# Kernel tuning notes

Hardware: AMD Instinct MI355X
Metric: run time of the kernel (lower is better)

## Reference

```python
import jax, jax.numpy as jnp
import numpy as np

H = 8  # heads hardcoded in LightGFormer


def layernorm(x, g, b, eps=1e-5):
    m = x.mean(-1, keepdims=True)
    v = ((x - m) ** 2).mean(-1, keepdims=True)
    return (x - m) / jnp.sqrt(v + eps) * g + b


def setup_inputs() -> dict:
    key = jax.random.key(0)
    B, N, D, L = 16, 512, 256, 4
    Dff = 4 * D
    ks = jax.random.split(key, 12)

    def w(k, shape, scale=0.02):
        return jax.random.normal(k, shape, jnp.float32) * scale

    return {
        "input": w(ks[0], (B, N, D), 1.0),
        "input_v": w(ks[1], (B, N, D), 1.0),
        "pos_emb": w(ks[2], (N, D)),
        "Wq": w(ks[3], (L, D, D)), "bq": jnp.zeros((L, D), jnp.float32),
        "Wk": w(ks[4], (L, D, D)), "bk": jnp.zeros((L, D), jnp.float32),
        "Wv": w(ks[5], (L, D, D)), "bv": jnp.zeros((L, D), jnp.float32),
        "Wo": w(ks[6], (L, D, D)), "bo": jnp.zeros((L, D), jnp.float32),
        "W1": w(ks[7], (L, D, Dff)), "b1": jnp.zeros((L, Dff), jnp.float32),
        "W2": w(ks[8], (L, Dff // 2, D // 2)), "b2": jnp.zeros((L, D // 2), jnp.float32),
        "g1": jnp.ones((L, D), jnp.float32), "be1": jnp.zeros((L, D), jnp.float32),
        "g2": jnp.ones((L, D), jnp.float32), "be2": jnp.zeros((L, D), jnp.float32),
        "gf": jnp.ones((D,), jnp.float32), "bf": jnp.zeros((D,), jnp.float32),
        "mask": jax.random.randint(ks[9], (N, N), 0, 2) > 0,
    }


def reference(input, input_v, pos_emb, Wq, bq, Wk, bk, Wv, bv, Wo, bo,
              W1, b1, W2, b2, g1, be1, g2, be2, gf, bf, mask):
    B, N, D = input.shape
    L = Wq.shape[0]
    dk = D // H
    scale = 1.0 / float(np.sqrt(dk))

    x = input + pos_emb[None]       # learned positional encoding
    xv = input_v + pos_emb[None]    # values stream (never updated across layers)

    for i in range(L):
        # --- self-attention: queries/keys from x, values from xv ---
        q = (x @ Wq[i] + bq[i]).reshape(B, N, H, dk)
        k = (x @ Wk[i] + bk[i]).reshape(B, N, H, dk)
        v = (xv @ Wv[i] + bv[i]).reshape(B, N, H, dk)
        att = jnp.einsum('bqhd,bkhd->bhqk', q, k) * scale
        if i % 2 == 1:  # odd layers use the mask (Lightformer alternation)
            att = jnp.where(mask[None, None], -jnp.inf, att)
        att = jax.nn.softmax(att, axis=-1)
        o = jnp.einsum('bhqk,bkhd->bqhd', att, v).reshape(B, N, D)
        o = o @ Wo[i] + bo[i]
        x = layernorm(x + o, g1[i], be1[i])
        # --- FFN with grouped second linear: [.., 2, 2D] @ [2D, D/2] ---
        h = jax.nn.gelu(x @ W1[i] + b1[i], approximate=False)
        h = (h.reshape(B, N, 2, 2 * D) @ W2[i] + b2[i]).reshape(B, N, D)
        x = layernorm(x + h, g2[i], be2[i])

    x = layernorm(x, gf, bf)  # final attention_norm
    return x
```

## Files before the change

kernel.cpp:

```cpp
#include <hip/hip_runtime.h>
#include <hip/hip_bf16.h>
#include <math.h>

#define BDIM 16
#define NSEQ 512
#define DMODEL 256
#define NLAYER 4
#define NHEAD 8
#define DK 32
#define DFF 1024
#define BN (BDIM * NSEQ)
#define ND (NSEQ * DMODEL)

typedef __bf16 bf16x8 __attribute__((ext_vector_type(8)));
typedef float floatx4 __attribute__((ext_vector_type(4)));
typedef unsigned uint32x2 __attribute__((ext_vector_type(2)));

static __device__ __forceinline__ unsigned short f2bf(float f) {
    unsigned u = __float_as_uint(f);
    unsigned r = (u + 0x7FFFu + ((u >> 16) & 1u)) >> 16;
    return (unsigned short)r;
}
static __device__ __forceinline__ float bf2f(unsigned short u) {
    return __uint_as_float(((unsigned)u) << 16);
}

static __device__ __forceinline__ void async_ld16(const unsigned short* g,
                                                  unsigned short* l) {
    __builtin_amdgcn_global_load_lds(
        (const __attribute__((address_space(1))) unsigned int*)g,
        (__attribute__((address_space(3))) unsigned int*)l, 16, 0, 0);
}

static __device__ __forceinline__ float gelu_f(float c) {
    float u = 0.7978845608028654f * (c + 0.044715f * c * c * c);
    return c * (1.f / (1.f + __expf(-2.f * u)));
}

static __device__ __forceinline__ unsigned cvtpk(float lo, float hi) {
    unsigned r;
    asm("v_cvt_pk_bf16_f32 %0, %1, %2" : "=v"(r) : "v"(lo), "v"(hi));
    return r;
}

__global__ void conv_all_kernel(const float* __restrict__ Wq, const float* __restrict__ Wk,
                                const float* __restrict__ Wv, const float* __restrict__ Wo,
                                const float* __restrict__ W1, const float* __restrict__ W2,
                                const int* __restrict__ mask,
                                unsigned short* __restrict__ wqT, unsigned short* __restrict__ wkT,
                                unsigned short* __restrict__ wvT,
                                unsigned short* __restrict__ wo_s,
                                unsigned short* __restrict__ w1_s, unsigned short* __restrict__ w2_s,
                                unsigned* __restrict__ bits) {
    int blk = blockIdx.x, tid = threadIdx.x;
    if (blk < 3072) {
        int i = blk * 256 + tid;
        int sel = i >> 18;
        int j = i & 262143;
        int l = j >> 16, rem = j & 65535, kk = rem >> 8, n = rem & 255;
        const float* src = sel == 0 ? Wq : sel == 1 ? Wk : Wv;
        unsigned short* dst = sel == 0 ? wqT : sel == 1 ? wkT : wvT;
        dst[(size_t)l * 65536 + n * 256 + kk] = f2bf(src[j]);
    } else if (blk < 4096) {
        int i = (blk - 3072) * 256 + tid;
        int l = i >> 16, o = i & 65535;
        int j = o & 7, quad = (o >> 3) & 3, l16 = (o >> 5) & 15;
        int kt = (o >> 9) & 7, cg = (o >> 12) & 15;
        int k = kt * 32 + (j >> 2) * 16 + quad * 4 + (j & 3);
        int dout = cg * 16 + l16;
        wo_s[(size_t)l * 65536 + o] = f2bf(Wo[(size_t)l * 65536 + k * 256 + dout]);
    } else if (blk < 8192) {
        int i = (blk - 4096) * 256 + tid;
        int l = i >> 18, o = i & 262143;
        int j = o & 7, quad = (o >> 3) & 3, l16 = (o >> 5) & 15;
        int kt = (o >> 9) & 7, cg = (o >> 12) & 63;
        int k = kt * 32 + (j >> 2) * 16 + quad * 4 + (j & 3);
        int dout = cg * 16 + l16;
        w1_s[(size_t)l * 262144 + o] = f2bf(W1[(size_t)l * 262144 + k * 1024 + dout]);
    } else if (blk < 9216) {
        int i = (blk - 8192) * 256 + tid;
        int l = i >> 16, o = i & 65535;
        int j = o & 7, quad = (o >> 3) & 3, l16 = (o >> 5) & 15;
        int kt = (o >> 9) & 15, cg = (o >> 13) & 7;
        int k = kt * 32 + (j >> 2) * 16 + quad * 4 + (j & 3);
        int dout = cg * 16 + l16;
        w2_s[(size_t)l * 65536 + o] = f2bf(W2[(size_t)l * 65536 + k * 128 + dout]);
    } else {
        int w = (blk - 9216) * 256 + tid;
        int r = w >> 4, wi = w & 15;
        const int* src = mask + r * NSEQ + wi * 32;
        unsigned acc = 0;
#pragma unroll
        for (int j = 0; j < 32; j++) acc |= (src[j] != 0 ? 1u : 0u) << j;
        bits[w] = acc;
    }
}

__global__ void add_pos_kernel(const float* __restrict__ in,
                               const float* __restrict__ inv,
                               const float* __restrict__ pos,
                               float* __restrict__ x,
                               unsigned short* __restrict__ xb,
                               unsigned short* __restrict__ xvb,
                               int total) {
    int i = blockIdx.x * blockDim.x + threadIdx.x;
    if (i < total) {
        float pe = pos[i % ND];
        float a = in[i] + pe;
        float b = inv[i] + pe;
        x[i] = a;
        xb[i] = f2bf(a);
        xvb[i] = f2bf(b);
    }
}

__global__ __launch_bounds__(256) void qkv_mfma_kernel(
        const unsigned short* __restrict__ xb,
        const unsigned short* __restrict__ xvb,
        const unsigned short* __restrict__ WqT, const unsigned short* __restrict__ WkT,
        const unsigned short* __restrict__ WvT,
        const float* __restrict__ bq, const float* __restrict__ bk,
        const float* __restrict__ bv,
        unsigned short* __restrict__ qo, unsigned short* __restrict__ ko,
        unsigned short* __restrict__ vo) {
    int proj = blockIdx.x >> 1;
    const unsigned short* A  = (proj == 2) ? xvb : xb;
    const unsigned short* Bt = (proj == 0) ? WqT : (proj == 1) ? WkT : WvT;
    const float* bias        = (proj == 0) ? bq  : (proj == 1) ? bk  : bv;
    unsigned short* Cb       = (proj == 0) ? qo  : (proj == 1) ? ko  : vo;
    float qscale = (proj == 0) ? 0.17677669529663687f : 1.f;

    __shared__ unsigned short As[128 * 32];
    __shared__ unsigned short Bs[128 * 32];
    int tid = threadIdx.x;
    int wave = tid >> 6, lane = tid & 63;
    int rowBase = blockIdx.y * 128, colBase = (blockIdx.x & 1) * 128;
    int m0w = (wave & 1) * 64, n0w = (wave >> 1) * 64;
    int lr = lane & 15, quad = lane >> 4;
    int qx = quad ^ (lr & 3);

    floatx4 acc[4][4];
#pragma unroll
    for (int mi = 0; mi < 4; mi++)
#pragma unroll
        for (int nj = 0; nj < 4; nj++) acc[mi][nj] = (floatx4)0.0f;

    for (int kt = 0; kt < DMODEL; kt += 32) {
#pragma unroll
        for (int t = 0; t < 2; t++) {
            int idx = t * 256 + tid;
            int row = idx >> 2, kv8 = ((idx ^ row) & 3) * 8;
            async_ld16(A + (size_t)(rowBase + row) * DMODEL + kt + kv8, &As[idx * 8]);
            async_ld16(Bt + (size_t)(colBase + row) * DMODEL + kt + kv8, &Bs[idx * 8]);
        }
        __syncthreads();
        bf16x8 af[4], bfr[4];
#pragma unroll
        for (int mi = 0; mi < 4; mi++)
            af[mi] = *(const bf16x8*)&As[(m0w + mi * 16 + lr) * 32 + qx * 8];
#pragma unroll
        for (int nj = 0; nj < 4; nj++)
            bfr[nj] = *(const bf16x8*)&Bs[(n0w + nj * 16 + lr) * 32 + qx * 8];
#pragma unroll
        for (int mi = 0; mi < 4; mi++)
#pragma unroll
            for (int nj = 0; nj < 4; nj++)
                acc[mi][nj] = __builtin_amdgcn_mfma_f32_16x16x32_bf16(
                    af[mi], bfr[nj], acc[mi][nj], 0, 0, 0);
        __syncthreads();
    }

#pragma unroll
    for (int mi = 0; mi < 4; mi++) {
#pragma unroll
        for (int r = 0; r < 4; r++) {
            int grow = rowBase + m0w + mi * 16 + quad * 4 + r;
#pragma unroll
            for (int nj = 0; nj < 4; nj++) {
                int gcol = colBase + n0w + nj * 16 + lr;
                float c = (acc[mi][nj][r] + bias[gcol]) * qscale;
                size_t off = ((size_t)((grow >> 9) * 8 + (gcol >> 5)) << 14)
                           + (size_t)(grow & 511) * 32 + (gcol & 31);
                Cb[off] = f2bf(c);
            }
        }
    }
}

__global__ __launch_bounds__(512, 4) void ffn_fused_kernel(
        const unsigned short* __restrict__ ab_f,
        const unsigned short* __restrict__ wo_s,
        const unsigned short* __restrict__ w1_s,
        const unsigned short* __restrict__ w2_s,
        const float* __restrict__ bo,
        const float* __restrict__ g1, const float* __restrict__ be1,
        const float* __restrict__ b1,
        const float* __restrict__ b2,
        const float* __restrict__ g2, const float* __restrict__ be2,
        const float* __restrict__ gf, const float* __restrict__ bf_,
        float* __restrict__ xf, unsigned short* __restrict__ xb,
        float* __restrict__ outF, int finalize) {
    __shared__ unsigned short X1s[8 * 512];
    __shared__ unsigned short Hs[16 * 512];
    __shared__ float redA[16][8], redB[16][8];
    __shared__ float redC[16][8], redD[16][8];
    __shared__ float redE[16][8], redF[16][8];

    int tid = threadIdx.x;
    int w = tid >> 6, lane = tid & 63, l16 = lane & 15, quad = lane >> 4;
    int bid = blockIdx.x;
    int rowBase = bid * 16;
    int fo = (l16 * 4 + quad) * 8;

#define TR2(d0, d1, addr)                                                  \
    asm volatile("ds_read_b64_tr_b16 %0, %2\n\t"                           \
                 "ds_read_b64_tr_b16 %1, %2 offset:512"                    \
                 : "=&v"(d0), "=&v"(d1) : "v"(addr))

    float bo_r[2], g1_r[2], be1_r[2], g2_r[2], be2_r[2], gf_r[2], bfr_[2];
#pragma unroll
    for (int cg = 0; cg < 2; cg++) {
        int colA = w * 32 + cg * 16 + l16;
        bo_r[cg] = bo[colA]; g1_r[cg] = g1[colA]; be1_r[cg] = be1[colA];
        int colC = cg * 128 + w * 16 + l16;
        g2_r[cg] = g2[colC]; be2_r[cg] = be2[colC];
        gf_r[cg] = gf[colC]; bfr_[cg] = bf_[colC];
    }
    float b1_r[2][4];
#pragma unroll
    for (int g = 0; g < 2; g++)
#pragma unroll
        for (int c = 0; c < 4; c++)
            b1_r[g][c] = b1[g * 512 + w * 64 + c * 16 + l16];
    float b2_r = b2[w * 16 + l16];
    float x0r[4][2];
#pragma unroll
    for (int r = 0; r < 4; r++)
#pragma unroll
        for (int cg = 0; cg < 2; cg++)
            x0r[r][cg] = xf[(size_t)(rowBase + quad * 4 + r) * 256 + w * 32 + cg * 16 + l16];

    floatx4 accA[2];
    accA[0] = (floatx4)0.0f; accA[1] = (floatx4)0.0f;

    bf16x8 afQ[4], bwQ[4][2];
#pragma unroll
    for (int p = 0; p < 4; p++) {
        afQ[p] = *(const bf16x8*)(ab_f + ((size_t)bid * 8 + p) * 512 + fo);
#pragma unroll
        for (int cg = 0; cg < 2; cg++)
            bwQ[p][cg] = *(const bf16x8*)(wo_s + ((size_t)((w * 2 + cg) * 8 + p)) * 512 + fo);
    }

#pragma unroll
    for (int kt = 0; kt < 8; kt++) {
        int sl = kt & 3;
#pragma unroll
        for (int cg = 0; cg < 2; cg++)
            accA[cg] = __builtin_amdgcn_mfma_f32_16x16x32_bf16(afQ[sl], bwQ[sl][cg], accA[cg], 0, 0, 0);
        if (kt < 4) {
            afQ[sl] = *(const bf16x8*)(ab_f + ((size_t)bid * 8 + kt + 4) * 512 + fo);
#pragma unroll
            for (int cg = 0; cg < 2; cg++)
                bwQ[sl][cg] = *(const bf16x8*)(wo_s + ((size_t)((w * 2 + cg) * 8 + kt + 4)) * 512 + fo);
        }
    }

#pragma unroll
    for (int r = 0; r < 4; r++) {
        int tok = quad * 4 + r;
        float s = 0.f, s2 = 0.f;
#pragma unroll
        for (int cg = 0; cg < 2; cg++) {
            float v = accA[cg][r] + bo_r[cg] + x0r[r][cg];
            accA[cg][r] = v; s += v; s2 += v * v;
        }
#pragma unroll
        for (int off = 1; off <= 8; off <<= 1) {
            s += __shfl_xor(s, off);
            s2 += __shfl_xor(s2, off);
        }
        if (l16 == 0) { redA[tok][w] = s; redB[tok][w] = s2; }
    }
    __syncthreads();
#pragma unroll
    for (int r = 0; r < 4; r++) {
        int tok = quad * 4 + r;
        float ts = 0.f, tq = 0.f;
#pragma unroll
        for (int ww = 0; ww < 8; ww++) { ts += redA[tok][ww]; tq += redB[tok][ww]; }
        float mean = ts * (1.f / 256.f);
        float var = tq * (1.f / 256.f) - mean * mean;
        float rstd = rsqrtf(var + 1e-5f);
#pragma unroll
        for (int cg = 0; cg < 2; cg++)
            accA[cg][r] = (accA[cg][r] - mean) * rstd * g1_r[cg] + be1_r[cg];
    }
#pragma unroll
    for (int cg = 0; cg < 2; cg++) {
        uint32x2 pk;
        pk[0] = cvtpk(accA[cg][0], accA[cg][1]);
        pk[1] = cvtpk(accA[cg][2], accA[cg][3]);
        *(uint32x2*)&X1s[w * 512 + (cg * 16 + l16) * 16 + quad * 4] = pk;
    }
    __syncthreads();

    unsigned x1addr = (unsigned)(size_t)&X1s[0] + (unsigned)(lane * 8);
    unsigned haddr  = (unsigned)(size_t)&Hs[0]  + (unsigned)(lane * 8);

    floatx4 y[2];
    y[0] = (floatx4)0.0f; y[1] = (floatx4)0.0f;

#pragma unroll
    for (int g = 0; g < 2; g++) {
        floatx4 accB[4];
#pragma unroll
        for (int c = 0; c < 4; c++) accB[c] = (floatx4)0.0f;

        uint32x2 tA0, tA1, tB0, tB1;
        TR2(tA0, tA1, x1addr);
        TR2(tB0, tB1, x1addr + 1024u);
        bf16x8 bwB[2][4];
#pragma unroll
        for (int p = 0; p < 2; p++)
#pragma unroll
            for (int c = 0; c < 4; c++)
                bwB[p][c] = *(const bf16x8*)(w1_s +
                    ((size_t)((g * 32 + w * 4 + c) * 8 + p)) * 512 + fo);

#pragma unroll
        for (int kt = 0; kt < 8; kt++) {
            if (kt < 7) asm volatile("s_waitcnt lgkmcnt(2)");
            else        asm volatile("s_waitcnt lgkmcnt(0)");
            __builtin_amdgcn_sched_barrier(0);
            union { bf16x8 v8; uint32x2 u[2]; } afu;
            if ((kt & 1) == 0) { afu.u[0] = tA0; afu.u[1] = tA1; }
            else               { afu.u[0] = tB0; afu.u[1] = tB1; }
            if (kt < 6) {
                if ((kt & 1) == 0) TR2(tA0, tA1, x1addr + (unsigned)((kt + 2) * 1024));
                else               TR2(tB0, tB1, x1addr + (unsigned)((kt + 2) * 1024));
            }
            int sl = kt & 1;
#pragma unroll
            for (int c = 0; c < 4; c++)
                accB[c] = __builtin_amdgcn_mfma_f32_16x16x32_bf16(afu.v8, bwB[sl][c], accB[c], 0, 0, 0);
            if (kt < 6) {
#pragma unroll
                for (int c = 0; c < 4; c++)
                    bwB[sl][c] = *(const bf16x8*)(w1_s +
                        ((size_t)((g * 32 + w * 4 + c) * 8 + kt + 2)) * 512 + fo);
            }
        }
#pragma unroll
        for (int c = 0; c < 4; c++) {
            float bb = b1_r[g][c];
            float o0 = gelu_f(accB[c][0] + bb);
            float o1 = gelu_f(accB[c][1] + bb);
            float o2 = gelu_f(accB[c][2] + bb);
            float o3 = gelu_f(accB[c][3] + bb);
            int ct = w * 2 + (c >> 1), colL = (c & 1) * 16 + l16;
            uint32x2 pk;
            pk[0] = cvtpk(o0, o1);
            pk[1] = cvtpk(o2, o3);
            *(uint32x2*)&Hs[ct * 512 + colL * 16 + quad * 4] = pk;
        }
        __syncthreads();

        TR2(tA0, tA1, haddr);
        TR2(tB0, tB1, haddr + 1024u);
        bf16x8 bwC[4];
#pragma unroll
        for (int p = 0; p < 4; p++)
            bwC[p] = *(const bf16x8*)(w2_s + ((size_t)(w * 16 + p)) * 512 + fo);

#pragma unroll
        for (int kt = 0; kt < 16; kt++) {
            if (kt < 15) asm volatile("s_waitcnt lgkmcnt(2)");
            else         asm volatile("s_waitcnt lgkmcnt(0)");
            __builtin_amdgcn_sched_barrier(0);
            union { bf16x8 v8; uint32x2 u[2]; } afu;
            if ((kt & 1) == 0) { afu.u[0] = tA0; afu.u[1] = tA1; }
            else               { afu.u[0] = tB0; afu.u[1] = tB1; }
            if (kt < 14) {
                if ((kt & 1) == 0) TR2(tA0, tA1, haddr + (unsigned)((kt + 2) * 1024));
                else               TR2(tB0, tB1, haddr + (unsigned)((kt + 2) * 1024));
            }
            y[g] = __builtin_amdgcn_mfma_f32_16x16x32_bf16(afu.v8, bwC[kt & 3], y[g], 0, 0, 0);
            if (kt < 12)
                bwC[kt & 3] = *(const bf16x8*)(w2_s + ((size_t)(w * 16 + kt + 4)) * 512 + fo);
        }
        if (g == 0) __syncthreads();
    }
#undef TR2

#pragma unroll
    for (int r = 0; r < 4; r++) {
        int tok = quad * 4 + r;
        float s = 0.f, s2 = 0.f;
#pragma unroll
        for (int g = 0; g < 2; g++) {
            int col = g * 128 + w * 16 + l16;
            float x1v = bf2f(X1s[(col >> 5) * 512 + (col & 31) * 16 + tok]);
            float v = y[g][r] + b2_r + x1v;
            y[g][r] = v; s += v; s2 += v * v;
        }
#pragma unroll
        for (int off = 1; off <= 8; off <<= 1) {
            s += __shfl_xor(s, off);
            s2 += __shfl_xor(s2, off);
        }
        if (l16 == 0) { redC[tok][w] = s; redD[tok][w] = s2; }
    }
    __syncthreads();

    if (!finalize) {
#pragma unroll
        for (int r = 0; r < 4; r++) {
            int tok = quad * 4 + r;
            float ts = 0.f, tq = 0.f;
#pragma unroll
            for (int ww = 0; ww < 8; ww++) { ts += redC[tok][ww]; tq += redD[tok][ww]; }
            float mean = ts * (1.f / 256.f);
            float var = tq * (1.f / 256.f) - mean * mean;
            float rstd = rsqrtf(var + 1e-5f);
#pragma unroll
            for (int g = 0; g < 2; g++) {
                int col = g * 128 + w * 16 + l16;
                float o = (y[g][r] - mean) * rstd * g2_r[g] + be2_r[g];
                xf[(size_t)(rowBase + tok) * 256 + col] = o;
                xb[(size_t)(rowBase + tok) * 256 + col] = f2bf(o);
            }
        }
    } else {
#pragma unroll
        for (int r = 0; r < 4; r++) {
            int tok = quad * 4 + r;
            float ts = 0.f, tq = 0.f;
#pragma unroll
            for (int ww = 0; ww < 8; ww++) { ts += redC[tok][ww]; tq += redD[tok][ww]; }
            float mean = ts * (1.f / 256.f);
            float var = tq * (1.f / 256.f) - mean * mean;
            float rstd = rsqrtf(var + 1e-5f);
            float s3 = 0.f, q3 = 0.f;
#pragma unroll
            for (int g = 0; g < 2; g++) {
                float o = (y[g][r] - mean) * rstd * g2_r[g] + be2_r[g];
                y[g][r] = o; s3 += o; q3 += o * o;
            }
#pragma unroll
            for (int off = 1; off <= 8; off <<= 1) {
                s3 += __shfl_xor(s3, off);
                q3 += __shfl_xor(q3, off);
            }
            if (l16 == 0) { redE[tok][w] = s3; redF[tok][w] = q3; }
        }
        __syncthreads();
#pragma unroll
        for (int r = 0; r < 4; r++) {
            int tok = quad * 4 + r;
            float ts = 0.f, tq = 0.f;
#pragma unroll
            for (int ww = 0; ww < 8; ww++) { ts += redE[tok][ww]; tq += redF[tok][ww]; }
            float mean = ts * (1.f / 256.f);
            float var = tq * (1.f / 256.f) - mean * mean;
            float rstd = rsqrtf(var + 1e-5f);
#pragma unroll
            for (int g = 0; g < 2; g++) {
                int col = g * 128 + w * 16 + l16;
                outF[(size_t)(rowBase + tok) * 256 + col]
                    = (y[g][r] - mean) * rstd * gf_r[g] + bfr_[g];
            }
        }
    }
}

__global__ __launch_bounds__(256, 4) void attn_mfma_kernel(
        const unsigned short* __restrict__ q, const unsigned short* __restrict__ k,
        const unsigned short* __restrict__ v, unsigned short* __restrict__ ab_f,
        const unsigned* __restrict__ mbits_g, int use_mask) {
    int bid = blockIdx.x;
    int qg = bid >> 7;
    int bh = bid & 127;
    int h = bh & 7, b = bh >> 3;
    int tid = threadIdx.x;

    __shared__ unsigned short Vs[2][NSEQ * 16];

    const unsigned short* kbase = k + (size_t)(b * 8 + h) * (NSEQ * DK);
    const unsigned short* vbase = v + (size_t)(b * 8 + h) * (NSEQ * DK);

#pragma unroll
    for (int db = 0; db < 2; db++) {
#pragma unroll
        for (int t = 0; t < 4; t++) {
            int c = t * 256 + tid;
            int kk = c >> 1, half = c & 1;
            async_ld16(vbase + (size_t)kk * 32 + db * 16 + half * 8,
                       &Vs[db][c * 8]);
        }
    }

    int wave = tid >> 6, lane = tid & 63, l16 = lane & 15, quad = lane >> 4;
    int qbase = qg * 64 + wave * 16;

    bf16x8 qf = *(const bf16x8*)(q + ((size_t)(b * 8 + h) * NSEQ + qbase + l16) * 32 + quad * 8);

    unsigned mw[16];
    if (use_mask) {
        const uint4* mr = (const uint4*)(mbits_g + (size_t)(qbase + l16) * 16);
#pragma unroll
        for (int w = 0; w < 4; w++) *(uint4*)&mw[w * 4] = mr[w];
    } else {
#pragma unroll
        for (int w = 0; w < 16; w++) mw[w] = 0;
    }
    __syncthreads();

    unsigned va0 = (unsigned)(size_t)&Vs[0][0] + (unsigned)(lane * 8);
    unsigned va1 = (unsigned)(size_t)&Vs[1][0] + (unsigned)(lane * 8);

    const unsigned short* kfrag = kbase + (size_t)l16 * DK + quad * 8;

    floatx4 oT0 = (floatx4)0.f, oT1 = (floatx4)0.f;
    float m_run = -INFINITY, l_part = 0.f;

    uint32x2 t00, t01, t02, t03, t10, t11, t12, t13;
#define TR_ISSUE8(cp)                                                      \
    asm volatile("ds_read_b64_tr_b16 %0, %8\n\t"                           \
                 "ds_read_b64_tr_b16 %1, %8 offset:512\n\t"                \
                 "ds_read_b64_tr_b16 %2, %8 offset:1024\n\t"               \
                 "ds_read_b64_tr_b16 %3, %8 offset:1536\n\t"               \
                 "ds_read_b64_tr_b16 %4, %9\n\t"                           \
                 "ds_read_b64_tr_b16 %5, %9 offset:512\n\t"                \
                 "ds_read_b64_tr_b16 %6, %9 offset:1024\n\t"               \
                 "ds_read_b64_tr_b16 %7, %9 offset:1536"                   \
                 : "=&v"(t00), "=&v"(t01), "=&v"(t02), "=&v"(t03),         \
                   "=&v"(t10), "=&v"(t11), "=&v"(t12), "=&v"(t13)          \
                 : "v"(va0 + (unsigned)((cp) * 2048)),                     \
                   "v"(va1 + (unsigned)((cp) * 2048)))
    TR_ISSUE8(0);

    bf16x8 k0 = *(const bf16x8*)(kfrag);
    bf16x8 k1 = *(const bf16x8*)(kfrag + 16 * DK);
    bf16x8 k2 = *(const bf16x8*)(kfrag + 32 * DK);
    bf16x8 k3 = *(const bf16x8*)(kfrag + 48 * DK);

#pragma unroll
    for (int cp = 0; cp < 8; cp++) {
        floatx4 s0 = __builtin_amdgcn_mfma_f32_16x16x32_bf16(k0, qf, (floatx4)0.f, 0, 0, 0);
        floatx4 s1 = __builtin_amdgcn_mfma_f32_16x16x32_bf16(k1, qf, (floatx4)0.f, 0, 0, 0);
        floatx4 s2 = __builtin_amdgcn_mfma_f32_16x16x32_bf16(k2, qf, (floatx4)0.f, 0, 0, 0);
        floatx4 s3 = __builtin_amdgcn_mfma_f32_16x16x32_bf16(k3, qf, (floatx4)0.f, 0, 0, 0);

        bf16x8 k0n, k1n, k2n, k3n;
        if (cp < 7) {
            const unsigned short* kn = kfrag + (size_t)((cp + 1) * 64) * DK;
            k0n = *(const bf16x8*)(kn);
            k1n = *(const bf16x8*)(kn + 16 * DK);
            k2n = *(const bf16x8*)(kn + 32 * DK);
            k3n = *(const bf16x8*)(kn + 48 * DK);
        }

        float sv[16];
#pragma unroll
        for (int r = 0; r < 4; r++) {
            sv[r] = s0[r]; sv[4 + r] = s1[r];
            sv[8 + r] = s2[r]; sv[12 + r] = s3[r];
        }
        if (use_mask) {
            unsigned wb0 = mw[2 * cp], wb1 = mw[2 * cp + 1];
#pragma unroll
            for (int r = 0; r < 4; r++) {
                if ((wb0 >> (quad * 4 + r)) & 1)        sv[r]      = -INFINITY;
                if ((wb0 >> (16 + quad * 4 + r)) & 1)   sv[4 + r]  = -INFINITY;
                if ((wb1 >> (quad * 4 + r)) & 1)        sv[8 + r]  = -INFINITY;
                if ((wb1 >> (16 + quad * 4 + r)) & 1)   sv[12 + r] = -INFINITY;
            }
        }
        float mx = sv[0];
#pragma unroll
        for (int j = 1; j < 16; j++) mx = fmaxf(mx, sv[j]);
        mx = fmaxf(mx, __shfl_xor(mx, 16));
        mx = fmaxf(mx, __shfl_xor(mx, 32));
        if (!__all(mx <= m_run)) {
            float mnew = fmaxf(m_run, mx);
            float corr = (m_run == mnew) ? 1.f : __expf(m_run - mnew);
            l_part *= corr;
            oT0 *= corr; oT1 *= corr;
            m_run = mnew;
        }
        float p[16];
#pragma unroll
        for (int j = 0; j < 16; j++) {
            float e = __expf(sv[j] - m_run);
            p[j] = (sv[j] > -INFINITY) ? e : 0.f;
            l_part += p[j];
        }
        union { bf16x8 v8; unsigned u[4]; } pf0, pf1;
#pragma unroll
        for (int j = 0; j < 4; j++) {
            pf0.u[j] = cvtpk(p[2 * j], p[2 * j + 1]);
            pf1.u[j] = cvtpk(p[8 + 2 * j], p[8 + 2 * j + 1]);
        }

        asm volatile("s_waitcnt lgkmcnt(0)");
        __builtin_amdgcn_sched_barrier(0);
        union { bf16x8 v8; uint32x2 u[2]; } av0, av1, av2, av3;
        av0.u[0] = t00; av0.u[1] = t01;
        av2.u[0] = t02; av2.u[1] = t03;
        av1.u[0] = t10; av1.u[1] = t11;
        av3.u[0] = t12; av3.u[1] = t13;

        oT0 = __builtin_amdgcn_mfma_f32_16x16x32_bf16(av0.v8, pf0.v8, oT0, 0, 0, 0);
        oT1 = __builtin_amdgcn_mfma_f32_16x16x32_bf16(av1.v8, pf0.v8, oT1, 0, 0, 0);
        oT0 = __builtin_amdgcn_mfma_f32_16x16x32_bf16(av2.v8, pf1.v8, oT0, 0, 0, 0);
        oT1 = __builtin_amdgcn_mfma_f32_16x16x32_bf16(av3.v8, pf1.v8, oT1, 0, 0, 0);
        if (cp < 7) TR_ISSUE8(cp + 1);
        k0 = k0n; k1 = k1n; k2 = k2n; k3 = k3n;
    }
#undef TR_ISSUE8

    float l = l_part;
    l += __shfl_xor(l, 16);
    l += __shfl_xor(l, 32);
    float invl = (l > 0.f) ? 1.f / l : 0.f;

    uint4 val;
    val.x = cvtpk(oT0[0] * invl, oT0[1] * invl);
    val.y = cvtpk(oT0[2] * invl, oT0[3] * invl);
    val.z = cvtpk(oT1[0] * invl, oT1[1] * invl);
    val.w = cvtpk(oT1[2] * invl, oT1[3] * invl);
    size_t panel = (size_t)b * 32 + qg * 4 + wave;
    *(uint4*)(ab_f + (panel * 8 + h) * 512 + (l16 * 4 + quad) * 8) = val;
}

extern "C" void kernel_launch(void* const* d_in, const int* in_sizes, int n_in,
                              void* d_out, int out_size, void* d_ws, size_t ws_size,
                              hipStream_t stream) {
    const float* input  = (const float*)d_in[0];
    const float* inputv = (const float*)d_in[1];
    const float* pos    = (const float*)d_in[2];
    const float* Wq = (const float*)d_in[3];
    const float* bq = (const float*)d_in[4];
    const float* Wk = (const float*)d_in[5];
    const float* bk = (const float*)d_in[6];
    const float* Wv = (const float*)d_in[7];
    const float* bv = (const float*)d_in[8];
    const float* Wo = (const float*)d_in[9];
    const float* bo = (const float*)d_in[10];
    const float* W1 = (const float*)d_in[11];
    const float* b1 = (const float*)d_in[12];
    const float* W2 = (const float*)d_in[13];
    const float* b2 = (const float*)d_in[14];
    const float* g1 = (const float*)d_in[15];
    const float* be1 = (const float*)d_in[16];
    const float* g2 = (const float*)d_in[17];
    const float* be2 = (const float*)d_in[18];
    const float* gf = (const float*)d_in[19];
    const float* bff = (const float*)d_in[20];
    const int* mask = (const int*)d_in[21];

    float* out = (float*)d_out;

    char* wsb = (char*)d_ws;
    float* x_f  = (float*)(wsb + ((size_t)0 << 20));
    unsigned short* x_b  = (unsigned short*)(wsb + ((size_t)8 << 20));
    unsigned short* xv_b = (unsigned short*)(wsb + ((size_t)12 << 20));
    unsigned short* qb_b = (unsigned short*)(wsb + ((size_t)16 << 20));
    unsigned short* kb_b = (unsigned short*)(wsb + ((size_t)20 << 20));
    unsigned short* vb_b = (unsigned short*)(wsb + ((size_t)24 << 20));
    unsigned short* ab_f = (unsigned short*)(wsb + ((size_t)28 << 20));
    unsigned short* wqT = (unsigned short*)(wsb + ((size_t)32 << 20));
    unsigned short* wkT = wqT + (size_t)4 * 65536;
    unsigned short* wvT = wkT + (size_t)4 * 65536;
    unsigned short* wo_s = wvT + (size_t)4 * 65536;
    unsigned short* w1_s = wo_s + (size_t)4 * 65536;
    unsigned short* w2_s = w1_s + (size_t)4 * 262144;
    unsigned* mbits = (unsigned*)(wsb + ((size_t)37 << 20));

    const size_t TOK = (size_t)BN * DMODEL;

    conv_all_kernel<<<9248, 256, 0, stream>>>(Wq, Wk, Wv, Wo, W1, W2, mask,
                                              wqT, wkT, wvT, wo_s, w1_s, w2_s, mbits);
    add_pos_kernel<<<(int)((TOK + 255) / 256), 256, 0, stream>>>(
        input, inputv, pos, x_f, x_b, xv_b, (int)TOK);

    for (int i = 0; i < NLAYER; i++) {
        const unsigned short* WqT_i = wqT + (size_t)i * 65536;
        const unsigned short* WkT_i = wkT + (size_t)i * 65536;
        const unsigned short* WvT_i = wvT + (size_t)i * 65536;
        const unsigned short* Wo_i  = wo_s + (size_t)i * 65536;
        const unsigned short* W1_i  = w1_s + (size_t)i * 262144;
        const unsigned short* W2_i  = w2_s + (size_t)i * 65536;

        qkv_mfma_kernel<<<dim3(6, 64), 256, 0, stream>>>(
            x_b, xv_b, WqT_i, WkT_i, WvT_i,
            bq + i * DMODEL, bk + i * DMODEL, bv + i * DMODEL,
            qb_b, kb_b, vb_b);

        attn_mfma_kernel<<<BDIM * NHEAD * 8, 256, 0, stream>>>(
            qb_b, kb_b, vb_b, ab_f, mbits, (i & 1));

        ffn_fused_kernel<<<BN / 16, 512, 0, stream>>>(
            ab_f, Wo_i, W1_i, W2_i,
            bo + i * DMODEL, g1 + i * DMODEL, be1 + i * DMODEL,
            b1 + i * DFF, b2 + i * (DMODEL / 2),
            g2 + i * DMODEL, be2 + i * DMODEL,
            gf, bff, x_f, x_b, out, (i == NLAYER - 1) ? 1 : 0);
    }
}
```

Before: 376.2 us.

## Store activations and QKV weights in MFMA fragment layout and drop LDS staging

Activations (x_b, xv_b) and the Q/K/V weights are now written in a pre-swizzled MFMA fragment order. This lets the QKV projection load operands straight from global memory into registers, with no LDS staging and no barriers. The QKV kernel moves from 128x128 tiles to one 16-token panel per block, giving 1536 blocks with a register double-buffered K loop. The cost is that every block re-reads its weight columns from L2, and the FFN epilogue now does an extra pass, including a redundant zero write, to scatter x_b in the new layout.

```diff
diff --git a/kernel.cpp b/kernel.cpp
--- a/kernel.cpp
+++ b/kernel.cpp
@@ -43,12 +43,20 @@
     return r;
 }
 
+static __device__ __forceinline__ size_t fd_addr(int tok, int col) {
+    int panel = tok >> 4, l16 = tok & 15;
+    int kt = col >> 5, kp = col & 31;
+    int quad = (kp >> 2) & 3;
+    int j = (kp & 3) + 4 * ((kp >> 4) & 1);
+    return ((size_t)(panel * 8 + kt) << 9) + (l16 * 4 + quad) * 8 + j;
+}
+
 __global__ void conv_all_kernel(const float* __restrict__ Wq, const float* __restrict__ Wk,
                                 const float* __restrict__ Wv, const float* __restrict__ Wo,
                                 const float* __restrict__ W1, const float* __restrict__ W2,
                                 const int* __restrict__ mask,
-                                unsigned short* __restrict__ wqT, unsigned short* __restrict__ wkT,
-                                unsigned short* __restrict__ wvT,
+                                unsigned short* __restrict__ wq_s, unsigned short* __restrict__ wk_s,
+                                unsigned short* __restrict__ wv_s,
                                 unsigned short* __restrict__ wo_s,
                                 unsigned short* __restrict__ w1_s, unsigned short* __restrict__ w2_s,
                                 unsigned* __restrict__ bits) {
@@ -56,11 +64,15 @@
     if (blk < 3072) {
         int i = blk * 256 + tid;
         int sel = i >> 18;
-        int j = i & 262143;
-        int l = j >> 16, rem = j & 65535, kk = rem >> 8, n = rem & 255;
+        int jj = i & 262143;
+        int l = jj >> 16, o = jj & 65535;
+        int j = o & 7, quad = (o >> 3) & 3, l16 = (o >> 5) & 15;
+        int kt = (o >> 9) & 7, cg = (o >> 12) & 15;
+        int k = kt * 32 + (j >> 2) * 16 + quad * 4 + (j & 3);
+        int dout = cg * 16 + l16;
         const float* src = sel == 0 ? Wq : sel == 1 ? Wk : Wv;
-        unsigned short* dst = sel == 0 ? wqT : sel == 1 ? wkT : wvT;
-        dst[(size_t)l * 65536 + n * 256 + kk] = f2bf(src[j]);
+        unsigned short* dst = sel == 0 ? wq_s : sel == 1 ? wk_s : wv_s;
+        dst[(size_t)l * 65536 + o] = f2bf(src[(size_t)l * 65536 + k * 256 + dout]);
     } else if (blk < 4096) {
         int i = (blk - 3072) * 256 + tid;
         int l = i >> 16, o = i & 65535;
@@ -109,80 +121,71 @@
         float a = in[i] + pe;
         float b = inv[i] + pe;
         x[i] = a;
-        xb[i] = f2bf(a);
-        xvb[i] = f2bf(b);
+        size_t fa = fd_addr(i >> 8, i & 255);
+        xb[fa] = f2bf(a);
+        xvb[fa] = f2bf(b);
     }
 }
 
 __global__ __launch_bounds__(256) void qkv_mfma_kernel(
-        const unsigned short* __restrict__ xb,
-        const unsigned short* __restrict__ xvb,
-        const unsigned short* __restrict__ WqT, const unsigned short* __restrict__ WkT,
-        const unsigned short* __restrict__ WvT,
+        const unsigned short* __restrict__ xb_f,
+        const unsigned short* __restrict__ xvb_f,
+        const unsigned short* __restrict__ wq_s, const unsigned short* __restrict__ wk_s,
+        const unsigned short* __restrict__ wv_s,
         const float* __restrict__ bq, const float* __restrict__ bk,
         const float* __restrict__ bv,
         unsigned short* __restrict__ qo, unsigned short* __restrict__ ko,
         unsigned short* __restrict__ vo) {
-    int proj = blockIdx.x >> 1;
-    const unsigned short* A  = (proj == 2) ? xvb : xb;
-    const unsigned short* Bt = (proj == 0) ? WqT : (proj == 1) ? WkT : WvT;
+    int bx = blockIdx.x;
+    int proj = bx >> 9, panel = bx & 511;
+    const unsigned short* A  = (proj == 2) ? xvb_f : xb_f;
+    const unsigned short* W  = (proj == 0) ? wq_s : (proj == 1) ? wk_s : wv_s;
     const float* bias        = (proj == 0) ? bq  : (proj == 1) ? bk  : bv;
     unsigned short* Cb       = (proj == 0) ? qo  : (proj == 1) ? ko  : vo;
     float qscale = (proj == 0) ? 0.17677669529663687f : 1.f;
 
-    __shared__ unsigned short As[128 * 32];
-    __shared__ unsigned short Bs[128 * 32];
     int tid = threadIdx.x;
-    int wave = tid >> 6, lane = tid & 63;
-    int rowBase = blockIdx.y * 128, colBase = (blockIdx.x & 1) * 128;
-    int m0w = (wave & 1) * 64, n0w = (wave >> 1) * 64;
-    int lr = lane & 15, quad = lane >> 4;
-    int qx = quad ^ (lr & 3);
-
-    floatx4 acc[4][4];
-#pragma unroll
-    for (int mi = 0; mi < 4; mi++)
-#pragma unroll
-        for (int nj = 0; nj < 4; nj++) acc[mi][nj] = (floatx4)0.0f;
-
-    for (int kt = 0; kt < DMODEL; kt += 32) {
-#pragma unroll
-        for (int t = 0; t < 2; t++) {
-            int idx = t * 256 + tid;
-            int row = idx >> 2, kv8 = ((idx ^ row) & 3) * 8;
-            async_ld16(A + (size_t)(rowBase + row) * DMODEL + kt + kv8, &As[idx * 8]);
-            async_ld16(Bt + (size_t)(colBase + row) * DMODEL + kt + kv8, &Bs[idx * 8]);
-        }
-        __syncthreads();
-        bf16x8 af[4], bfr[4];
-#pragma unroll
-        for (int mi = 0; mi < 4; mi++)
-            af[mi] = *(const bf16x8*)&As[(m0w + mi * 16 + lr) * 32 + qx * 8];
-#pragma unroll
-        for (int nj = 0; nj < 4; nj++)
-            bfr[nj] = *(const bf16x8*)&Bs[(n0w + nj * 16 + lr) * 32 + qx * 8];
-#pragma unroll
-        for (int mi = 0; mi < 4; mi++)
-#pragma unroll
-            for (int nj = 0; nj < 4; nj++)
-                acc[mi][nj] = __builtin_amdgcn_mfma_f32_16x16x32_bf16(
-                    af[mi], bfr[nj], acc[mi][nj], 0, 0, 0);
-        __syncthreads();
-    }
-
-#pragma unroll
-    for (int mi = 0; mi < 4; mi++) {
+    int w = tid >> 6, lane = tid & 63, l16 = lane & 15, quad = lane >> 4;
+    int fo = (l16 * 4 + quad) * 8;
+
+    floatx4 acc[4];
+#pragma unroll
+    for (int cg = 0; cg < 4; cg++) acc[cg] = (floatx4)0.0f;
+
+    bf16x8 afQ[4], bwQ[4][4];
+#pragma unroll
+    for (int p = 0; p < 4; p++) {
+        afQ[p] = *(const bf16x8*)(A + ((size_t)panel * 8 + p) * 512 + fo);
+#pragma unroll
+        for (int cg = 0; cg < 4; cg++)
+            bwQ[p][cg] = *(const bf16x8*)(W + ((size_t)((w * 4 + cg) * 8 + p)) * 512 + fo);
+    }
+
+#pragma unroll
+    for (int kt = 0; kt < 8; kt++) {
+        int sl = kt & 3;
+#pragma unroll
+        for (int cg = 0; cg < 4; cg++)
+            acc[cg] = __builtin_amdgcn_mfma_f32_16x16x32_bf16(afQ[sl], bwQ[sl][cg], acc[cg], 0, 0, 0);
+        if (kt < 4) {
+            afQ[sl] = *(const bf16x8*)(A + ((size_t)panel * 8 + kt + 4) * 512 + fo);
+#pragma unroll
+            for (int cg = 0; cg < 4; cg++)
+                bwQ[sl][cg] = *(const bf16x8*)(W + ((size_t)((w * 4 + cg) * 8 + kt + 4)) * 512 + fo);
+        }
+    }
+
+#pragma unroll
+    for (int cg = 0; cg < 4; cg++) {
+        int gcol = w * 64 + cg * 16 + l16;
+        float bb = bias[gcol];
 #pragma unroll
         for (int r = 0; r < 4; r++) {
-            int grow = rowBase + m0w + mi * 16 + quad * 4 + r;
-#pragma unroll
-            for (int nj = 0; nj < 4; nj++) {
-                int gcol = colBase + n0w + nj * 16 + lr;
-                float c = (acc[mi][nj][r] + bias[gcol]) * qscale;
-                size_t off = ((size_t)((grow >> 9) * 8 + (gcol >> 5)) << 14)
-                           + (size_t)(grow & 511) * 32 + (gcol & 31);
-                Cb[off] = f2bf(c);
-            }
+            int grow = panel * 16 + quad * 4 + r;
+            float c = (acc[cg][r] + bb) * qscale;
+            size_t off = ((size_t)((grow >> 9) * 8 + (gcol >> 5)) << 14)
+                       + (size_t)(grow & 511) * 32 + (gcol & 31);
+            Cb[off] = f2bf(c);
         }
     }
 }
@@ -428,7 +431,26 @@
                 int col = g * 128 + w * 16 + l16;
                 float o = (y[g][r] - mean) * rstd * g2_r[g] + be2_r[g];
                 xf[(size_t)(rowBase + tok) * 256 + col] = o;
-                xb[(size_t)(rowBase + tok) * 256 + col] = f2bf(o);
+                xb[((size_t)(bid * 8 + (col >> 5)) << 9) + fd_addr(tok, col) % 512
+                   + 0] = 0;
+            }
+        }
+#pragma unroll
+        for (int r = 0; r < 4; r++) {
+            int tok = quad * 4 + r;
+            float ts = 0.f, tq = 0.f;
+#pragma unroll
+            for (int ww = 0; ww < 8; ww++) { ts += redC[tok][ww]; tq += redD[tok][ww]; }
+            float mean = ts * (1.f / 256.f);
+            float var = tq * (1.f / 256.f) - mean * mean;
+            float rstd = rsqrtf(var + 1e-5f);
+#pragma unroll
+            for (int g = 0; g < 2; g++) {
+                int col = g * 128 + w * 16 + l16;
+                float o = (y[g][r] - mean) * rstd * g2_r[g] + be2_r[g];
+                int kp = col & 31;
+                int qk = (kp >> 2) & 3, jk = (kp & 3) + 4 * ((kp >> 4) & 1);
+                xb[((size_t)(bid * 8 + (col >> 5)) << 9) + (tok * 4 + qk) * 8 + jk] = f2bf(o);
             }
         }
     } else {
@@ -670,10 +692,10 @@
     unsigned short* kb_b = (unsigned short*)(wsb + ((size_t)20 << 20));
     unsigned short* vb_b = (unsigned short*)(wsb + ((size_t)24 << 20));
     unsigned short* ab_f = (unsigned short*)(wsb + ((size_t)28 << 20));
-    unsigned short* wqT = (unsigned short*)(wsb + ((size_t)32 << 20));
-    unsigned short* wkT = wqT + (size_t)4 * 65536;
-    unsigned short* wvT = wkT + (size_t)4 * 65536;
-    unsigned short* wo_s = wvT + (size_t)4 * 65536;
+    unsigned short* wq_s = (unsigned short*)(wsb + ((size_t)32 << 20));
+    unsigned short* wk_s = wq_s + (size_t)4 * 65536;
+    unsigned short* wv_s = wk_s + (size_t)4 * 65536;
+    unsigned short* wo_s = wv_s + (size_t)4 * 65536;
     unsigned short* w1_s = wo_s + (size_t)4 * 65536;
     unsigned short* w2_s = w1_s + (size_t)4 * 262144;
     unsigned* mbits = (unsigned*)(wsb + ((size_t)37 << 20));
@@ -681,20 +703,20 @@
     const size_t TOK = (size_t)BN * DMODEL;
 
     conv_all_kernel<<<9248, 256, 0, stream>>>(Wq, Wk, Wv, Wo, W1, W2, mask,
-                                              wqT, wkT, wvT, wo_s, w1_s, w2_s, mbits);
+                                              wq_s, wk_s, wv_s, wo_s, w1_s, w2_s, mbits);
     add_pos_kernel<<<(int)((TOK + 255) / 256), 256, 0, stream>>>(
         input, inputv, pos, x_f, x_b, xv_b, (int)TOK);
 
     for (int i = 0; i < NLAYER; i++) {
-        const unsigned short* WqT_i = wqT + (size_t)i * 65536;
-        const unsigned short* WkT_i = wkT + (size_t)i * 65536;
-        const unsigned short* WvT_i = wvT + (size_t)i * 65536;
-        const unsigned short* Wo_i  = wo_s + (size_t)i * 65536;
-        const unsigned short* W1_i  = w1_s + (size_t)i * 262144;
-        const unsigned short* W2_i  = w2_s + (size_t)i * 65536;
-
-        qkv_mfma_kernel<<<dim3(6, 64), 256, 0, stream>>>(
-            x_b, xv_b, WqT_i, WkT_i, WvT_i,
+        const unsigned short* Wq_i = wq_s + (size_t)i * 65536;
+        const unsigned short* Wk_i = wk_s + (size_t)i * 65536;
+        const unsigned short* Wv_i = wv_s + (size_t)i * 65536;
+        const unsigned short* Wo_i = wo_s + (size_t)i * 65536;
+        const unsigned short* W1_i = w1_s + (size_t)i * 262144;
+        const unsigned short* W2_i = w2_s + (size_t)i * 65536;
+
+        qkv_mfma_kernel<<<1536, 256, 0, stream>>>(
+            x_b, xv_b, Wq_i, Wk_i, Wv_i,
             bq + i * DMODEL, bk + i * DMODEL, bv + i * DMODEL,
             qb_b, kb_b, vb_b);
 
```

Result: slower. 406.9 us (+8.2%).

## Fuse both FFN1 column groups into one K loop and deepen FFN2 prefetch

Applied to the files above, without the earlier changes.

The first FFN matmul now computes all eight output column tiles in a single K loop, so each transposed LDS read of the X1 activation fragment feeds eight MFMAs instead of four and the A fragments are read once instead of twice. Weight fragments are loaded fresh each k-step rather than double-buffered across iterations. The second FFN matmul keeps four transposed LDS reads in flight and issues two MFMAs per step. This raises accumulator register pressure (eight floatx4 accumulators plus eight weight vectors live at once), which may hurt occupancy or cause spills.

```diff
diff --git a/kernel.cpp b/kernel.cpp
--- a/kernel.cpp
+++ b/kernel.cpp
@@ -311,25 +311,22 @@
     floatx4 y[2];
     y[0] = (floatx4)0.0f; y[1] = (floatx4)0.0f;
 
-#pragma unroll
-    for (int g = 0; g < 2; g++) {
-        floatx4 accB[4];
-#pragma unroll
-        for (int c = 0; c < 4; c++) accB[c] = (floatx4)0.0f;
-
+    floatx4 accB[8];
+#pragma unroll
+    for (int c = 0; c < 8; c++) accB[c] = (floatx4)0.0f;
+
+    {
         uint32x2 tA0, tA1, tB0, tB1;
         TR2(tA0, tA1, x1addr);
         TR2(tB0, tB1, x1addr + 1024u);
-        bf16x8 bwB[2][4];
-#pragma unroll
-        for (int p = 0; p < 2; p++)
-#pragma unroll
-            for (int c = 0; c < 4; c++)
-                bwB[p][c] = *(const bf16x8*)(w1_s +
-                    ((size_t)((g * 32 + w * 4 + c) * 8 + p)) * 512 + fo);
-
 #pragma unroll
         for (int kt = 0; kt < 8; kt++) {
+            bf16x8 bwB[8];
+#pragma unroll
+            for (int c = 0; c < 8; c++) {
+                int tile = ((c < 4) ? 0 : 32) + w * 4 + (c & 3);
+                bwB[c] = *(const bf16x8*)(w1_s + ((size_t)(tile * 8 + kt)) * 512 + fo);
+            }
             if (kt < 7) asm volatile("s_waitcnt lgkmcnt(2)");
             else        asm volatile("s_waitcnt lgkmcnt(0)");
             __builtin_amdgcn_sched_barrier(0);
@@ -340,24 +337,22 @@
                 if ((kt & 1) == 0) TR2(tA0, tA1, x1addr + (unsigned)((kt + 2) * 1024));
                 else               TR2(tB0, tB1, x1addr + (unsigned)((kt + 2) * 1024));
             }
-            int sl = kt & 1;
-#pragma unroll
-            for (int c = 0; c < 4; c++)
-                accB[c] = __builtin_amdgcn_mfma_f32_16x16x32_bf16(afu.v8, bwB[sl][c], accB[c], 0, 0, 0);
-            if (kt < 6) {
-#pragma unroll
-                for (int c = 0; c < 4; c++)
-                    bwB[sl][c] = *(const bf16x8*)(w1_s +
-                        ((size_t)((g * 32 + w * 4 + c) * 8 + kt + 2)) * 512 + fo);
-            }
-        }
+#pragma unroll
+            for (int c = 0; c < 8; c++)
+                accB[c] = __builtin_amdgcn_mfma_f32_16x16x32_bf16(afu.v8, bwB[c], accB[c], 0, 0, 0);
+        }
+    }
+
+#pragma unroll
+    for (int g = 0; g < 2; g++) {
 #pragma unroll
         for (int c = 0; c < 4; c++) {
             float bb = b1_r[g][c];
-            float o0 = gelu_f(accB[c][0] + bb);
-            float o1 = gelu_f(accB[c][1] + bb);
-            float o2 = gelu_f(accB[c][2] + bb);
-            float o3 = gelu_f(accB[c][3] + bb);
+            floatx4 a = accB[g * 4 + c];
+            float o0 = gelu_f(a[0] + bb);
+            float o1 = gelu_f(a[1] + bb);
+            float o2 = gelu_f(a[2] + bb);
+            float o3 = gelu_f(a[3] + bb);
             int ct = w * 2 + (c >> 1), colL = (c & 1) * 16 + l16;
             uint32x2 pk;
             pk[0] = cvtpk(o0, o1);
@@ -366,28 +361,34 @@
         }
         __syncthreads();
 
-        TR2(tA0, tA1, haddr);
-        TR2(tB0, tB1, haddr + 1024u);
-        bf16x8 bwC[4];
-#pragma unroll
-        for (int p = 0; p < 4; p++)
-            bwC[p] = *(const bf16x8*)(w2_s + ((size_t)(w * 16 + p)) * 512 + fo);
-
-#pragma unroll
-        for (int kt = 0; kt < 16; kt++) {
-            if (kt < 15) asm volatile("s_waitcnt lgkmcnt(2)");
-            else         asm volatile("s_waitcnt lgkmcnt(0)");
-            __builtin_amdgcn_sched_barrier(0);
-            union { bf16x8 v8; uint32x2 u[2]; } afu;
-            if ((kt & 1) == 0) { afu.u[0] = tA0; afu.u[1] = tA1; }
-            else               { afu.u[0] = tB0; afu.u[1] = tB1; }
-            if (kt < 14) {
-                if ((kt & 1) == 0) TR2(tA0, tA1, haddr + (unsigned)((kt + 2) * 1024));
-                else               TR2(tB0, tB1, haddr + (unsigned)((kt + 2) * 1024));
-            }
-            y[g] = __builtin_amdgcn_mfma_f32_16x16x32_bf16(afu.v8, bwC[kt & 3], y[g], 0, 0, 0);
-            if (kt < 12)
-                bwC[kt & 3] = *(const bf16x8*)(w2_s + ((size_t)(w * 16 + kt + 4)) * 512 + fo);
+        {
+            uint32x2 u0, u1, u2, u3, u4, u5, u6, u7;
+            TR2(u0, u1, haddr);
+            TR2(u2, u3, haddr + 1024u);
+            TR2(u4, u5, haddr + 2048u);
+            TR2(u6, u7, haddr + 3072u);
+#pragma unroll
+            for (int it = 0; it < 8; it++) {
+                bf16x8 bw0 = *(const bf16x8*)(w2_s + ((size_t)(w * 16 + 2 * it)) * 512 + fo);
+                bf16x8 bw1 = *(const bf16x8*)(w2_s + ((size_t)(w * 16 + 2 * it + 1)) * 512 + fo);
+                if (it < 7) asm volatile("s_waitcnt lgkmcnt(4)");
+                else        asm volatile("s_waitcnt lgkmcnt(0)");
+                __builtin_amdgcn_sched_barrier(0);
+                union { bf16x8 v8; uint32x2 u[2]; } af0, af1;
+                if ((it & 1) == 0) { af0.u[0] = u0; af0.u[1] = u1; af1.u[0] = u2; af1.u[1] = u3; }
+                else               { af0.u[0] = u4; af0.u[1] = u5; af1.u[0] = u6; af1.u[1] = u7; }
+                if (it < 6) {
+                    if ((it & 1) == 0) {
+                        TR2(u0, u1, haddr + (unsigned)((2 * it + 4) * 1024));
+                        TR2(u2, u3, haddr + (unsigned)((2 * it + 5) * 1024));
+                    } else {
+                        TR2(u4, u5, haddr + (unsigned)((2 * it + 4) * 1024));
+                        TR2(u6, u7, haddr + (unsigned)((2 * it + 5) * 1024));
+                    }
+                }
+                y[g] = __builtin_amdgcn_mfma_f32_16x16x32_bf16(af0.v8, bw0, y[g], 0, 0, 0);
+                y[g] = __builtin_amdgcn_mfma_f32_16x16x32_bf16(af1.v8, bw1, y[g], 0, 0, 0);
+            }
         }
         if (g == 0) __syncthreads();
     }
```

New measurement: 384.4 us. +2.2%, slower.
